# Kernel optimization log

Measured on AMD Instinct MI355X. Metric: run time of the kernel, lower is better.

Reference implementation:

```python
import jax, jax.numpy as jnp
import numpy as np

N = 50000   # nodes
E = 600000  # edges (both relations mixed)
D = 128     # in_features == out_features


def _gcn(x, W, b, row, col, w, n):
    """PyG GCNConv: add self-loops (weight 1), symmetric normalization, linear, aggregate, bias.
    Edges with w==0 contribute nothing to degree or messages (== masked subgraph)."""
    idx = jnp.arange(n)
    srow = jnp.concatenate([row, idx])
    scol = jnp.concatenate([col, idx])
    sw = jnp.concatenate([w, jnp.ones((n,), x.dtype)])
    deg = jax.ops.segment_sum(sw, scol, num_segments=n)                 # [n]
    dinv = jnp.where(deg > 0, jax.lax.rsqrt(jnp.maximum(deg, 1e-12)), 0.0)
    norm = dinv[srow] * sw * dinv[scol]                                 # [E+n]
    h = x @ W                                                           # [n, D]
    out = jax.ops.segment_sum(h[srow] * norm[:, None], scol, num_segments=n)
    return out + b


def setup_inputs() -> dict:
    key = jax.random.key(0)
    ks = jax.random.split(key, 12)
    s_in = 1.0 / np.sqrt(D)
    s_g = 1.0 / np.sqrt(3 * D)
    return {
        "x": jax.random.normal(ks[0], (N, D), dtype=jnp.float32),
        "edge_index": jax.random.randint(ks[1], (2, E), 0, N, dtype=jnp.int64),
        "edge_type": jax.random.randint(ks[2], (E,), 0, 2, dtype=jnp.int64),
        "W_sl": jax.random.normal(ks[3], (D, D), dtype=jnp.float32) * s_in,
        "b_sl": jnp.zeros((D,), jnp.float32),
        "W0": jax.random.normal(ks[4], (D, D), dtype=jnp.float32) * s_in,
        "b0": jnp.zeros((D,), jnp.float32),
        "W1": jax.random.normal(ks[5], (D, D), dtype=jnp.float32) * s_in,
        "b1": jnp.zeros((D,), jnp.float32),
        "W_g": jax.random.normal(ks[6], (3 * D, D), dtype=jnp.float32) * s_g,
        "b_g": jnp.zeros((D,), jnp.float32),
    }


def reference(x, edge_index, edge_type, W_sl, b_sl, W0, b0, W1, b1, W_g, b_g):
    n = x.shape[0]
    row, col = edge_index[0], edge_index[1]
    x_x = x @ W_sl + b_sl                                   # self-loop linear
    w0 = (edge_type == 0).astype(x.dtype)
    w1 = (edge_type == 1).astype(x.dtype)
    x_n = _gcn(x, W0, b0, row, col, w0, n)                  # relation 0 GCN
    x_d = _gcn(x, W1, b1, row, col, w1, n)                  # relation 1 GCN
    gat_raw = jax.nn.softmax(jnp.concatenate([x_x, x_n, x_d], axis=1) @ W_g + b_g, axis=-1)
    gat = jnp.cumsum(gat_raw, axis=-1)                      # ordered-neuron gate
    return x_d[:, ::-1] * gat + x_x + x_n
```

## Files before the change

kernel.cpp:

```cpp
#include <hip/hip_runtime.h>
#include <hip/hip_bf16.h>
#include <hip/hip_fp16.h>
#include <math.h>


typedef __attribute__((ext_vector_type(8))) short bf16x8;
typedef __attribute__((ext_vector_type(4))) float f32x4;
typedef __attribute__((ext_vector_type(8))) unsigned short ushort8;

__device__ inline float b2f(unsigned short u) {
  return __uint_as_float(((unsigned)u) << 16);
}
__device__ inline unsigned short f2bf(float f) {
  __hip_bfloat16 b = __float2bfloat16(f);
  return *reinterpret_cast<unsigned short*>(&b);
}

__global__ __launch_bounds__(256) void pack_zero(const float* __restrict__ Wsl,
                                                 const float* __restrict__ W0,
                                                 const float* __restrict__ W1,
                                                 const float* __restrict__ Wg,
                                                 unsigned short* __restrict__ Wp3,
                                                 unsigned short* __restrict__ Wgp,
                                                 int4* __restrict__ deg4, int n4) {
  if (blockIdx.x < 48) {
    int tid = blockIdx.x * 256 + threadIdx.x;
    if (tid < 6144) {
      int z = tid / 2048, r = tid % 2048;
      int lane = r & 63, idx = r >> 6;
      int kf = idx & 3, ct = idx >> 2;
      const float* W = (z == 0) ? Wsl : (z == 1) ? W0 : W1;
      unsigned short* dst = Wp3 + (size_t)z * 16384 + (size_t)r * 8;
      int krow = kf * 32 + (lane >> 4) * 8;
      int ccol = ct * 16 + (lane & 15);
#pragma unroll
      for (int j = 0; j < 8; ++j) dst[j] = f2bf(W[(size_t)(krow + j) * 128 + ccol]);
    } else {
      int r = tid - 6144;
      int lane = r & 63, idx = r >> 6;
      int kf = idx % 12, ct = idx / 12;
      unsigned short* dst = Wgp + (size_t)r * 8;
      int krow = kf * 32 + (lane >> 4) * 8;
      int ccol = ct * 16 + (lane & 15);
#pragma unroll
      for (int j = 0; j < 8; ++j) dst[j] = f2bf(Wg[(size_t)(krow + j) * 128 + ccol]);
    }
  } else {
    int i = (blockIdx.x - 48) * 256 + threadIdx.x;
    if (i < n4) deg4[i] = make_int4(0, 0, 0, 0);
  }
}

__global__ __launch_bounds__(256) void count_gemm(
    const float* __restrict__ x, const unsigned short* __restrict__ Wp3,
    const float* __restrict__ bsl, unsigned short* __restrict__ hx,
    unsigned short* __restrict__ h0, unsigned short* __restrict__ h1,
    const int* __restrict__ col, const int* __restrict__ etype,
    int* __restrict__ deg, int* __restrict__ erank, int n, int E, int gb) {
  __shared__ unsigned short xs[64 * 136];
  __shared__ __align__(16) unsigned short Bs[2][4096];
  int tid = threadIdx.x;
  if ((int)blockIdx.x >= gb) {
    int e = (blockIdx.x - gb) * 256 + tid;
    if (e >= E) return;
    int rk = atomicAdd(&deg[(size_t)etype[e] * n + col[e]], 1);
    erank[e] = rk;
    return;
  }
  int row0 = blockIdx.x * 64;
  {
    const float4* xg = (const float4*)(x + (size_t)row0 * 128);
    int maxv = (n - row0) * 32;
#pragma unroll
    for (int i = 0; i < 8; ++i) {
      int idx = tid + i * 256;
      float4 v = {0.f, 0.f, 0.f, 0.f};
      if (idx < maxv) v = xg[idx];
      int rr = idx >> 5, c4 = idx & 31;
      ushort4 u;
      u.x = f2bf(v.x);
      u.y = f2bf(v.y);
      u.z = f2bf(v.z);
      u.w = f2bf(v.w);
      *(ushort4*)&xs[rr * 136 + c4 * 4] = u;
    }
    int u = tid;
#pragma unroll
    for (int r = 0; r < 2; ++r, u += 256) {
      int ct = u >> 6, ll = u & 63;
      *(ushort8*)&Bs[0][u * 8] = *(const ushort8*)(Wp3 + ((size_t)(ct * 4) * 64 + ll) * 8);
    }
  }
  __syncthreads();
  int w = tid >> 6;
  int l = tid & 63;
  int q = l >> 4;
  int c = l & 15;
  bf16x8 af[4];
#pragma unroll
  for (int kf = 0; kf < 4; ++kf)
    af[kf] = *(const bf16x8*)&xs[(w * 16 + c) * 136 + kf * 32 + q * 8];
  __syncthreads();

  f32x4 acc[8];
#pragma unroll
  for (int ct = 0; ct < 8; ++ct) acc[ct] = (f32x4){0.f, 0.f, 0.f, 0.f};
#pragma unroll
  for (int g = 0; g < 12; ++g) {
    int z = g >> 2, kf = g & 3;
    int cur = g & 1;
    if (g < 11) {
      int zn = (g + 1) >> 2, kfn = (g + 1) & 3;
      int u = tid;
#pragma unroll
      for (int r = 0; r < 2; ++r, u += 256) {
        int ct = u >> 6, ll = u & 63;
        *(ushort8*)&Bs[cur ^ 1][u * 8] = *(const ushort8*)(
            Wp3 + (size_t)zn * 16384 + ((size_t)(ct * 4 + kfn) * 64 + ll) * 8);
      }
    }
    bf16x8 a = af[kf];
#pragma unroll
    for (int ct = 0; ct < 8; ++ct)
      acc[ct] = __builtin_amdgcn_mfma_f32_16x16x32_bf16(
          a, *(const bf16x8*)&Bs[cur][(ct * 64 + l) * 8], acc[ct], 0, 0, 0);
    if (kf == 3) {
      unsigned short* h = (z == 0) ? hx : (z == 1) ? h0 : h1;
#pragma unroll
      for (int ct = 0; ct < 8; ++ct) {
        int fc = ct * 16 + c;
        float bias = (z == 0) ? bsl[fc] : 0.f;
#pragma unroll
        for (int i = 0; i < 4; ++i)
          xs[(w * 16 + q * 4 + i) * 136 + fc] = f2bf(acc[ct][i] + bias);
        acc[ct] = (f32x4){0.f, 0.f, 0.f, 0.f};
      }
      __syncthreads();
#pragma unroll
      for (int i = 0; i < 4; ++i) {
        int idx = tid + i * 256;
        int rr = idx >> 4, c8 = idx & 15;
        int gr = row0 + rr;
        if (gr < n)
          *(ushort8*)(h + (size_t)gr * 128 + c8 * 8) = *(const ushort8*)&xs[rr * 136 + c8 * 8];
      }
      __syncthreads();
    } else {
      __syncthreads();
    }
  }
}

__global__ __launch_bounds__(256) void scan1(const int* __restrict__ deg,
                                             int* __restrict__ partials, int n2) {
  int tid = threadIdx.x;
  int base = blockIdx.x * 2048 + tid * 8;
  int s = 0;
#pragma unroll
  for (int k = 0; k < 8; ++k) {
    int i = base + k;
    if (i < n2) s += deg[i];
  }
  __shared__ int sb[256];
  sb[tid] = s;
  __syncthreads();
  for (int o = 128; o; o >>= 1) {
    if (tid < o) sb[tid] += sb[tid + o];
    __syncthreads();
  }
  if (tid == 0) partials[blockIdx.x] = sb[0];
}

__global__ __launch_bounds__(256) void scan3b(const int* __restrict__ partials,
                                              const int* __restrict__ deg,
                                              int* __restrict__ row_start,
                                              float* __restrict__ dinv, int n2, int nb) {
  __shared__ int sb[256];
  __shared__ int ex[256];
  int tid = threadIdx.x;
  int pv = (tid < nb) ? partials[tid] : 0;
  sb[tid] = pv;
  __syncthreads();
  for (int o = 1; o < 256; o <<= 1) {
    int t = (tid >= o) ? sb[tid - o] : 0;
    __syncthreads();
    sb[tid] += t;
    __syncthreads();
  }
  ex[tid] = sb[tid] - pv;
  __syncthreads();
  int base = ex[blockIdx.x];
  __syncthreads();

  int bstart = blockIdx.x * 2048 + tid * 8;
  int v[8];
  int s = 0;
#pragma unroll
  for (int k = 0; k < 8; ++k) {
    int i = bstart + k;
    v[k] = (i < n2) ? deg[i] : 0;
    s += v[k];
    if (i < n2) dinv[i] = rsqrtf((float)v[k] + 1.0f);
  }
  sb[tid] = s;
  __syncthreads();
  for (int o = 1; o < 256; o <<= 1) {
    int t = (tid >= o) ? sb[tid - o] : 0;
    __syncthreads();
    sb[tid] += t;
    __syncthreads();
  }
  int run = base + (sb[tid] - s);
#pragma unroll
  for (int k = 0; k < 8; ++k) {
    int i = bstart + k;
    if (i < n2) {
      row_start[i] = run;
      run += v[k];
    }
  }
}

__global__ __launch_bounds__(256) void fill_k(const int* __restrict__ row,
                                              const int* __restrict__ col,
                                              const int* __restrict__ etype,
                                              const int* __restrict__ erank,
                                              const int* __restrict__ row_start,
                                              const float* __restrict__ dinv,
                                              unsigned int* __restrict__ ebuf,
                                              int n, int E) {
  int e = blockIdx.x * 256 + threadIdx.x;
  if (e >= E) return;
  int r = row[e], c = col[e], t = etype[e];
  int b = t * n + c;
  float nrm = dinv[t * n + r] * dinv[b];
  int pos = row_start[b] + erank[e];
  unsigned int rec = (unsigned int)(r & 0xFFFF) |
                     ((unsigned int)__half_as_ushort(__float2half_rn(nrm)) << 16);
  ebuf[pos] = rec;
}

__global__ __launch_bounds__(256) void gather2(const unsigned short* __restrict__ h0,
                                               const unsigned short* __restrict__ h1,
                                               const unsigned int* __restrict__ ebuf,
                                               const int* __restrict__ row_start,
                                               const int* __restrict__ deg,
                                               const float* __restrict__ dinv,
                                               const float* __restrict__ b0,
                                               const float* __restrict__ b1,
                                               unsigned short* __restrict__ xn,
                                               unsigned short* __restrict__ xd, int n) {
  int t = blockIdx.y;
  long long gid = (long long)blockIdx.x * 256 + threadIdx.x;
  int node = (int)(gid >> 3);
  if (node >= n) return;
  int sub = (int)(gid & 7);
  const ushort8* hp8 = (const ushort8*)(t ? h1 : h0);
  const float* bias = t ? b1 : b0;
  unsigned short* out = t ? xd : xn;
  const int* rs = row_start + (size_t)t * n;
  const int* dg = deg + (size_t)t * n;
  float di = dinv[(size_t)t * n + node];

  float accA[8], accB[8];
  float acc2A[8] = {0, 0, 0, 0, 0, 0, 0, 0}, acc2B[8] = {0, 0, 0, 0, 0, 0, 0, 0};
  {
    ushort8 sa = hp8[(size_t)node * 16 + sub * 2];
    ushort8 sbv = hp8[(size_t)node * 16 + sub * 2 + 1];
    float sl = di * di;
#pragma unroll
    for (int k = 0; k < 8; ++k) {
      accA[k] = fmaf(b2f(sa[k]), sl, bias[sub * 16 + k]);
      accB[k] = fmaf(b2f(sbv[k]), sl, bias[sub * 16 + 8 + k]);
    }
  }
  int s = rs[node];
  int e = s + dg[node];
  int j = s;
  for (; j + 3 < e; j += 4) {
    unsigned int r0 = ebuf[j], r1 = ebuf[j + 1], r2 = ebuf[j + 2], r3 = ebuf[j + 3];
    int i0 = (int)(r0 & 0xFFFFu), i1 = (int)(r1 & 0xFFFFu);
    int i2 = (int)(r2 & 0xFFFFu), i3 = (int)(r3 & 0xFFFFu);
    float n0 = __half2float(__ushort_as_half((unsigned short)(r0 >> 16)));
    float n1 = __half2float(__ushort_as_half((unsigned short)(r1 >> 16)));
    float n2 = __half2float(__ushort_as_half((unsigned short)(r2 >> 16)));
    float n3 = __half2float(__ushort_as_half((unsigned short)(r3 >> 16)));
    ushort8 v0a = hp8[(size_t)i0 * 16 + sub * 2];
    ushort8 v0b = hp8[(size_t)i0 * 16 + sub * 2 + 1];
    ushort8 v1a = hp8[(size_t)i1 * 16 + sub * 2];
    ushort8 v1b = hp8[(size_t)i1 * 16 + sub * 2 + 1];
    ushort8 v2a = hp8[(size_t)i2 * 16 + sub * 2];
    ushort8 v2b = hp8[(size_t)i2 * 16 + sub * 2 + 1];
    ushort8 v3a = hp8[(size_t)i3 * 16 + sub * 2];
    ushort8 v3b = hp8[(size_t)i3 * 16 + sub * 2 + 1];
#pragma unroll
    for (int k = 0; k < 8; ++k) {
      accA[k] = fmaf(b2f(v0a[k]), n0, accA[k]);
      accB[k] = fmaf(b2f(v0b[k]), n0, accB[k]);
      acc2A[k] = fmaf(b2f(v1a[k]), n1, acc2A[k]);
      acc2B[k] = fmaf(b2f(v1b[k]), n1, acc2B[k]);
      accA[k] = fmaf(b2f(v2a[k]), n2, accA[k]);
      accB[k] = fmaf(b2f(v2b[k]), n2, accB[k]);
      acc2A[k] = fmaf(b2f(v3a[k]), n3, acc2A[k]);
      acc2B[k] = fmaf(b2f(v3b[k]), n3, acc2B[k]);
    }
  }
  for (; j < e; ++j) {
    unsigned int r0 = ebuf[j];
    int i0 = (int)(r0 & 0xFFFFu);
    float n0 = __half2float(__ushort_as_half((unsigned short)(r0 >> 16)));
    ushort8 v0a = hp8[(size_t)i0 * 16 + sub * 2];
    ushort8 v0b = hp8[(size_t)i0 * 16 + sub * 2 + 1];
#pragma unroll
    for (int k = 0; k < 8; ++k) {
      accA[k] = fmaf(b2f(v0a[k]), n0, accA[k]);
      accB[k] = fmaf(b2f(v0b[k]), n0, accB[k]);
    }
  }
  ushort8 ua, ub;
#pragma unroll
  for (int k = 0; k < 8; ++k) {
    ua[k] = f2bf(accA[k] + acc2A[k]);
    ub[k] = f2bf(accB[k] + acc2B[k]);
  }
  ((ushort8*)out)[(size_t)node * 16 + sub * 2] = ua;
  ((ushort8*)out)[(size_t)node * 16 + sub * 2 + 1] = ub;
}

__global__ __launch_bounds__(256) void gate_combine(
    const unsigned short* __restrict__ hx, const unsigned short* __restrict__ xn,
    const unsigned short* __restrict__ xd, const unsigned short* __restrict__ Wgp,
    const float* __restrict__ bg, float* __restrict__ out, int n) {
  __shared__ __align__(16) unsigned short Bs[2][4096];
  int tid = threadIdx.x;
  int wv = tid >> 6;
  int l = tid & 63;
  int q = l >> 4;
  int c = l & 15;
  int row0 = blockIdx.x * 64 + wv * 16;
  int ar = row0 + c;
  if (ar > n - 1) ar = n - 1;
  bf16x8 af[12];
  {
    const unsigned short* p0 = hx + (size_t)ar * 128 + q * 8;
    const unsigned short* p1 = xn + (size_t)ar * 128 + q * 8;
    const unsigned short* p2 = xd + (size_t)ar * 128 + q * 8;
#pragma unroll
    for (int k = 0; k < 4; ++k) {
      af[k] = *(const bf16x8*)(p0 + k * 32);
      af[4 + k] = *(const bf16x8*)(p1 + k * 32);
      af[8 + k] = *(const bf16x8*)(p2 + k * 32);
    }
  }
  {
    int u = tid;
#pragma unroll
    for (int r = 0; r < 2; ++r, u += 256) {
      int ct = u >> 6, ll = u & 63;
      *(ushort8*)&Bs[0][u * 8] = *(const ushort8*)(Wgp + ((size_t)(ct * 12) * 64 + ll) * 8);
    }
  }
  __syncthreads();
  f32x4 acc[8];
#pragma unroll
  for (int ct = 0; ct < 8; ++ct) acc[ct] = (f32x4){0.f, 0.f, 0.f, 0.f};
#pragma unroll
  for (int kf = 0; kf < 12; ++kf) {
    int cur = kf & 1;
    if (kf < 11) {
      int u = tid;
#pragma unroll
      for (int r = 0; r < 2; ++r, u += 256) {
        int ct = u >> 6, ll = u & 63;
        *(ushort8*)&Bs[cur ^ 1][u * 8] =
            *(const ushort8*)(Wgp + ((size_t)(ct * 12 + kf + 1) * 64 + ll) * 8);
      }
    }
    bf16x8 a = af[kf];
#pragma unroll
    for (int ct = 0; ct < 8; ++ct)
      acc[ct] = __builtin_amdgcn_mfma_f32_16x16x32_bf16(
          a, *(const bf16x8*)&Bs[cur][(ct * 64 + l) * 8], acc[ct], 0, 0, 0);
    if (kf < 11) __syncthreads();
  }
#pragma unroll
  for (int ct = 0; ct < 8; ++ct) {
    float bgv = bg[ct * 16 + c];
#pragma unroll
    for (int i = 0; i < 4; ++i) acc[ct][i] += bgv;
  }
#pragma unroll
  for (int i = 0; i < 4; ++i) {
    float m = acc[0][i];
#pragma unroll
    for (int ct = 1; ct < 8; ++ct) m = fmaxf(m, acc[ct][i]);
#pragma unroll
    for (int o = 1; o < 16; o <<= 1) m = fmaxf(m, __shfl_xor(m, o));
    float e[8];
    float s = 0.f;
#pragma unroll
    for (int ct = 0; ct < 8; ++ct) {
      e[ct] = __expf(acc[ct][i] - m);
      s += e[ct];
    }
#pragma unroll
    for (int o = 1; o < 16; o <<= 1) s += __shfl_xor(s, o);
    float inv = 1.0f / s;
    int gr = row0 + q * 4 + i;
    float run = 0.f;
#pragma unroll
    for (int ct = 0; ct < 8; ++ct) {
      float p = e[ct];
#pragma unroll
      for (int o = 1; o < 16; o <<= 1) {
        float t = __shfl_up(p, o);
        if (c >= o) p += t;
      }
      float T = __shfl(p, q * 16 + 15);
      float gat = (run + p) * inv;
      run += T;
      int f = ct * 16 + c;
      if (gr < n) {
        size_t gb = (size_t)gr * 128;
        float xxv = b2f(hx[gb + f]);
        float xnv = b2f(xn[gb + f]);
        float xdv = b2f(xd[gb + 127 - f]);
        out[gb + f] = fmaf(xdv, gat, xxv + xnv);
      }
    }
  }
}

extern "C" void kernel_launch(void* const* d_in, const int* in_sizes, int n_in,
                              void* d_out, int out_size, void* d_ws, size_t ws_size,
                              hipStream_t stream) {
  const float* x = (const float*)d_in[0];
  const int* eidx = (const int*)d_in[1];
  const int* etype = (const int*)d_in[2];
  const float* Wsl = (const float*)d_in[3];
  const float* bsl = (const float*)d_in[4];
  const float* W0 = (const float*)d_in[5];
  const float* b0 = (const float*)d_in[6];
  const float* W1 = (const float*)d_in[7];
  const float* b1 = (const float*)d_in[8];
  const float* Wg = (const float*)d_in[9];
  const float* bg = (const float*)d_in[10];
  int n = in_sizes[0] / 128;
  int E = in_sizes[2];
  const int* row = eidx;
  const int* col = eidx + E;
  int n2 = 2 * n;

  char* w = (char*)d_ws;
  int* deg = (int*)w;             w += (size_t)n2 * 4;
  float* dinv = (float*)w;        w += (size_t)n2 * 4;
  int* row_start = (int*)w;       w += (size_t)n2 * 4;
  int* partials = (int*)w;        w += 1024;
  unsigned int* ebuf = (unsigned int*)w;  w += (size_t)E * 4;
  int* erank = (int*)w;           w += (size_t)E * 4;
  unsigned short* Wp3 = (unsigned short*)w;  w += 3 * 128 * 128 * 2;
  unsigned short* Wgp = (unsigned short*)w;  w += 384 * 128 * 2;
  unsigned short* hx = (unsigned short*)w;   w += (size_t)n * 128 * 2;
  unsigned short* h0 = (unsigned short*)w;   w += (size_t)n * 128 * 2;
  unsigned short* h1 = (unsigned short*)w;   w += (size_t)n * 128 * 2;
  unsigned short* xn = (unsigned short*)w;   w += (size_t)n * 128 * 2;
  unsigned short* xd = (unsigned short*)w;
  float* out = (float*)d_out;

  int n4 = n2 / 4;
  int zb = (n4 + 255) / 256;
  pack_zero<<<48 + zb, 256, 0, stream>>>(Wsl, W0, W1, Wg, Wp3, Wgp, (int4*)deg, n4);

  int cd_blocks = (E + 255) / 256;
  int gemm_blocks = (n + 63) / 64;
  count_gemm<<<gemm_blocks + cd_blocks, 256, 0, stream>>>(
      x, Wp3, bsl, hx, h0, h1, col, etype, deg, erank, n, E, gemm_blocks);

  int nb = (n2 + 2047) / 2048;
  scan1<<<nb, 256, 0, stream>>>(deg, partials, n2);
  scan3b<<<nb, 256, 0, stream>>>(partials, deg, row_start, dinv, n2, nb);

  fill_k<<<cd_blocks, 256, 0, stream>>>(row, col, etype, erank, row_start, dinv,
                                        ebuf, n, E);

  int ga_blocks = (int)(((long long)n * 8 + 255) / 256);
  gather2<<<dim3(ga_blocks, 2), 256, 0, stream>>>(h0, h1, ebuf, row_start, deg, dinv,
                                                  b0, b1, xn, xd, n);
  gate_combine<<<(n + 63) / 64, 256, 0, stream>>>(hx, xn, xd, Wgp, bg, out, n);
}
```

Baseline: 124.1 us.

## Split gather and gate into halves and overlap in a mixed kernel

The node range is split in two. The first half is gathered alone. A mixed kernel then runs the gate/combine for the first half alongside the gather for the second half, and a final kernel gates the second half. The aim is to let the compute-heavy gate work and the memory-bound gather overlap on the GPU. In exchange it adds a third launch and gives the gather blocks in the mixed kernel the gate's shared-memory footprint, which may lower their occupancy.

```diff
diff --git a/kernel.cpp b/kernel.cpp
--- a/kernel.cpp
+++ b/kernel.cpp
@@ -240,20 +240,16 @@
   ebuf[pos] = rec;
 }
 
-__global__ __launch_bounds__(256) void gather2(const unsigned short* __restrict__ h0,
-                                               const unsigned short* __restrict__ h1,
-                                               const unsigned int* __restrict__ ebuf,
-                                               const int* __restrict__ row_start,
-                                               const int* __restrict__ deg,
-                                               const float* __restrict__ dinv,
-                                               const float* __restrict__ b0,
-                                               const float* __restrict__ b1,
-                                               unsigned short* __restrict__ xn,
-                                               unsigned short* __restrict__ xd, int n) {
-  int t = blockIdx.y;
-  long long gid = (long long)blockIdx.x * 256 + threadIdx.x;
-  int node = (int)(gid >> 3);
-  if (node >= n) return;
+__device__ __forceinline__ void gather_body(
+    int tid, int vbid, int t, int node_base, int node_lim,
+    const unsigned short* __restrict__ h0, const unsigned short* __restrict__ h1,
+    const unsigned int* __restrict__ ebuf, const int* __restrict__ row_start,
+    const int* __restrict__ deg, const float* __restrict__ dinv,
+    const float* __restrict__ b0, const float* __restrict__ b1,
+    unsigned short* __restrict__ xn, unsigned short* __restrict__ xd, int n) {
+  long long gid = (long long)vbid * 256 + tid;
+  int node = node_base + (int)(gid >> 3);
+  if (node >= node_lim) return;
   int sub = (int)(gid & 7);
   const ushort8* hp8 = (const ushort8*)(t ? h1 : h0);
   const float* bias = t ? b1 : b0;
@@ -327,17 +323,17 @@
   ((ushort8*)out)[(size_t)node * 16 + sub * 2 + 1] = ub;
 }
 
-__global__ __launch_bounds__(256) void gate_combine(
+__device__ __forceinline__ void gate_body(
+    int tid, int vbid, int row_base, int row_lim,
     const unsigned short* __restrict__ hx, const unsigned short* __restrict__ xn,
     const unsigned short* __restrict__ xd, const unsigned short* __restrict__ Wgp,
-    const float* __restrict__ bg, float* __restrict__ out, int n) {
-  __shared__ __align__(16) unsigned short Bs[2][4096];
-  int tid = threadIdx.x;
+    const float* __restrict__ bg, float* __restrict__ out, int n,
+    unsigned short (*Bs)[4096]) {
   int wv = tid >> 6;
   int l = tid & 63;
   int q = l >> 4;
   int c = l & 15;
-  int row0 = blockIdx.x * 64 + wv * 16;
+  int row0 = row_base + vbid * 64 + wv * 16;
   int ar = row0 + c;
   if (ar > n - 1) ar = n - 1;
   bf16x8 af[12];
@@ -420,7 +416,7 @@
       float gat = (run + p) * inv;
       run += T;
       int f = ct * 16 + c;
-      if (gr < n) {
+      if (gr < row_lim) {
         size_t gb = (size_t)gr * 128;
         float xxv = b2f(hx[gb + f]);
         float xnv = b2f(xn[gb + f]);
@@ -429,6 +425,46 @@
       }
     }
   }
+}
+
+__global__ __launch_bounds__(256) void gather_k(
+    const unsigned short* __restrict__ h0, const unsigned short* __restrict__ h1,
+    const unsigned int* __restrict__ ebuf, const int* __restrict__ row_start,
+    const int* __restrict__ deg, const float* __restrict__ dinv,
+    const float* __restrict__ b0, const float* __restrict__ b1,
+    unsigned short* __restrict__ xn, unsigned short* __restrict__ xd,
+    int node_base, int node_lim, int n) {
+  gather_body(threadIdx.x, blockIdx.x, blockIdx.y, node_base, node_lim,
+              h0, h1, ebuf, row_start, deg, dinv, b0, b1, xn, xd, n);
+}
+
+__global__ __launch_bounds__(256) void mix_k(
+    const unsigned short* __restrict__ hx, const unsigned short* __restrict__ h0,
+    const unsigned short* __restrict__ h1, const unsigned int* __restrict__ ebuf,
+    const int* __restrict__ row_start, const int* __restrict__ deg,
+    const float* __restrict__ dinv, const float* __restrict__ b0,
+    const float* __restrict__ b1, const unsigned short* __restrict__ Wgp,
+    const float* __restrict__ bg, unsigned short* __restrict__ xn,
+    unsigned short* __restrict__ xd, float* __restrict__ out,
+    int gtb, int gab2, int nh, int n) {
+  __shared__ __align__(16) unsigned short Bs[2][4096];
+  if ((int)blockIdx.x < gtb) {
+    gate_body(threadIdx.x, blockIdx.x, 0, nh, hx, xn, xd, Wgp, bg, out, n, Bs);
+  } else {
+    int b = blockIdx.x - gtb;
+    int t = (b >= gab2) ? 1 : 0;
+    int vb = t ? b - gab2 : b;
+    gather_body(threadIdx.x, vb, t, nh, n, h0, h1, ebuf, row_start, deg, dinv,
+                b0, b1, xn, xd, n);
+  }
+}
+
+__global__ __launch_bounds__(256) void gate_k(
+    const unsigned short* __restrict__ hx, const unsigned short* __restrict__ xn,
+    const unsigned short* __restrict__ xd, const unsigned short* __restrict__ Wgp,
+    const float* __restrict__ bg, float* __restrict__ out, int row_base, int n) {
+  __shared__ __align__(16) unsigned short Bs[2][4096];
+  gate_body(threadIdx.x, blockIdx.x, row_base, n, hx, xn, xd, Wgp, bg, out, n, Bs);
 }
 
 extern "C" void kernel_launch(void* const* d_in, const int* in_sizes, int n_in,
@@ -483,8 +519,17 @@
   fill_k<<<cd_blocks, 256, 0, stream>>>(row, col, etype, erank, row_start, dinv,
                                         ebuf, n, E);
 
-  int ga_blocks = (int)(((long long)n * 8 + 255) / 256);
-  gather2<<<dim3(ga_blocks, 2), 256, 0, stream>>>(h0, h1, ebuf, row_start, deg, dinv,
-                                                  b0, b1, xn, xd, n);
-  gate_combine<<<(n + 63) / 64, 256, 0, stream>>>(hx, xn, xd, Wgp, bg, out, n);
-}
+  int nh = ((n / 2 + 63) / 64) * 64;
+  if (nh > n) nh = n;
+  int ga1 = (int)(((long long)nh * 8 + 255) / 256);
+  gather_k<<<dim3(ga1, 2), 256, 0, stream>>>(h0, h1, ebuf, row_start, deg, dinv,
+                                             b0, b1, xn, xd, 0, nh, n);
+  int gtb = nh / 64;
+  int gab2 = (int)(((long long)(n - nh) * 8 + 255) / 256);
+  mix_k<<<gtb + 2 * gab2, 256, 0, stream>>>(hx, h0, h1, ebuf, row_start, deg, dinv,
+                                            b0, b1, Wgp, bg, xn, xd, out,
+                                            gtb, gab2, nh, n);
+  int g2 = (n - nh + 63) / 64;
+  if (g2 > 0)
+    gate_k<<<g2, 256, 0, stream>>>(hx, xn, xd, Wgp, bg, out, nh, n);
+}
```

Result: slower. 137.8 us (+11.0%).
